# Optimization experiments

Hardware: AMD Instinct MI355X
Metric: run time of the kernel (lower is better)

Reference implementation:

```python
import jax, jax.numpy as jnp
import numpy as np

N = 8192
DIM = 128


def setup_inputs() -> dict:
    key = jax.random.key(0)
    k1, k2 = jax.random.split(key)
    mapping = jax.random.normal(k1, (N, DIM), dtype=jnp.float32)
    # Cost matrix of the finite metric: symmetric, strictly positive off-diagonal,
    # zero diagonal (the module adds eye to the denominator to handle the diagonal).
    Draw = jax.random.uniform(k2, (N, N), dtype=jnp.float32) * 2.0 + 0.1
    D = 0.5 * (Draw + Draw.T)
    D = D * (1.0 - jnp.eye(N, dtype=jnp.float32))
    return {"mapping": mapping, "D": D}


def reference(mapping, D):
    # Pairwise Euclidean distances via GEMM formulation (||a||^2 - 2ab + ||b||^2)
    # instead of materializing the O(N^2 * dim) broadcast difference.
    n = D.shape[0]
    sq = jnp.sum(mapping * mapping, axis=-1)               # [N]
    gram = mapping @ mapping.T                             # [N, N]
    d2 = sq[:, None] + sq[None, :] - 2.0 * gram            # [N, N]
    d2 = jnp.maximum(d2, 0.0)
    # safe sqrt (exact 0 on the diagonal, matching torch.norm forward)
    pos = d2 > 0
    d = jnp.sqrt(jnp.where(pos, d2, 1.0)) * pos
    ratio = jnp.abs(d - D) / (D + jnp.eye(n, dtype=D.dtype))
    return jnp.sum(ratio) / (n * n - n)
```

## Files before the change

### kernel.cpp

```cpp
#include <hip/hip_runtime.h>
#include <math.h>

#define NN 8192
#define DIM 128
#define TS 32
#define NSTRIP (NN / TS)
#define TOTTILES (NSTRIP * (NSTRIP + 1) / 2)
#define TPW 4
#define NWAVE (TOTTILES / TPW)
#define NBLOCKS (NWAVE / 4)

typedef short bf16x8 __attribute__((ext_vector_type(8)));
typedef float f32x4 __attribute__((ext_vector_type(4)));

__device__ inline unsigned short f2bf(float x) {
    unsigned u = __float_as_uint(x);
    unsigned r = u + 0x7FFFu + ((u >> 16) & 1u);
    return (unsigned short)(r >> 16);
}

__global__ void pack_kernel(const float* __restrict__ m, unsigned short* __restrict__ buf2) {
    const int t = threadIdx.x, l = t & 63;
    const int W = blockIdx.x * 4 + (t >> 6);
    const int g = W >> 2, kq = W & 3;
    const int row = g * 16 + (l & 15);
    const int k0 = kq * 32 + (l >> 4) * 8;
    const float* src = m + (size_t)row * DIM + k0;
    float4 v0 = *reinterpret_cast<const float4*>(src);
    float4 v1 = *reinterpret_cast<const float4*>(src + 4);
    float f[8] = {v0.x, v0.y, v0.z, v0.w, v1.x, v1.y, v1.z, v1.w};
    union { ushort4 u4[2]; unsigned short us[8]; } o;
#pragma unroll
    for (int q = 0; q < 8; ++q) o.us[q] = f2bf(f[q]);
    unsigned short* dst = buf2 + (size_t)W * 512 + l * 8;
    *reinterpret_cast<ushort4*>(dst) = o.u4[0];
    *reinterpret_cast<ushort4*>(dst + 4) = o.u4[1];
}

__global__ void sq_kernel(const float* __restrict__ mapping, float* __restrict__ sq) {
    int i = blockIdx.x * blockDim.x + threadIdx.x;
    if (i < NN) {
        const float4* row = reinterpret_cast<const float4*>(mapping + (size_t)i * DIM);
        float s = 0.f;
#pragma unroll
        for (int q = 0; q < DIM / 4; ++q) {
            float4 v = row[q];
            s += v.x * v.x + v.y * v.y + v.z * v.z + v.w * v.w;
        }
        sq[i] = s;
    }
}

__global__ __launch_bounds__(256, 3) void dist_kernel(const unsigned short* __restrict__ buf2,
                                                      const float* __restrict__ D,
                                                      const float* __restrict__ sq,
                                                      float* __restrict__ partials) {
    __shared__ float smem[4][1024];
    __shared__ float wred[4];

    const int t = threadIdx.x, l = t & 63, w = t >> 6;
    const int b = blockIdx.x;
    const int nb = (b & 7) * (NBLOCKS / 8) + (b >> 3);
    const int W = nb * 4 + w;

    int idx0 = __builtin_amdgcn_readfirstlane(W * TPW);
    int si = 0, base = 0;
    while (idx0 >= base + (NSTRIP - si)) { base += NSTRIP - si; ++si; }
    int cj = si + (idx0 - base);

    const int l15 = l & 15, l4 = l >> 4, l7 = l & 7, l3 = l >> 3;
    float* sm = smem[w];

    f32x4 dc[4];
#pragma unroll
    for (int k = 0; k < 4; ++k)
        dc[k] = *reinterpret_cast<const f32x4*>(
            D + (size_t)(si * TS + l3 + 8 * k) * NN + cj * TS + l7 * 4);

    bf16x8 af[2][4];
#pragma unroll
    for (int it = 0; it < 2; ++it)
#pragma unroll
        for (int kq = 0; kq < 4; ++kq)
            af[it][kq] = *(const bf16x8*)(buf2 + (size_t)((si * 2 + it) * 4 + kq) * 512 + l * 8);

    float tsum = 0.f;

#pragma unroll
    for (int tt = 0; tt < TPW; ++tt) {
        int nsi = si, ncj = cj + 1;
        if (ncj == NSTRIP) { nsi = si + 1; ncj = nsi; }
        if (tt == TPW - 1) { nsi = si; ncj = cj; }

        bf16x8 bf[2][4];
#pragma unroll
        for (int jt = 0; jt < 2; ++jt)
#pragma unroll
            for (int kq = 0; kq < 4; ++kq)
                bf[jt][kq] = *(const bf16x8*)(buf2 + (size_t)((cj * 2 + jt) * 4 + kq) * 512 + l * 8);
        float sqa[4];
#pragma unroll
        for (int k = 0; k < 4; ++k) sqa[k] = sq[si * TS + l3 + 8 * k];
        f32x4 sqb = *reinterpret_cast<const f32x4*>(sq + cj * TS + l7 * 4);

        f32x4 dn[4];
#pragma unroll
        for (int k = 0; k < 4; ++k)
            dn[k] = *reinterpret_cast<const f32x4*>(
                D + (size_t)(nsi * TS + l3 + 8 * k) * NN + ncj * TS + l7 * 4);
        __builtin_amdgcn_sched_barrier(0);

        f32x4 acc[2][2] = {};
#pragma unroll
        for (int kq = 0; kq < 4; ++kq)
#pragma unroll
            for (int it = 0; it < 2; ++it)
#pragma unroll
                for (int jt = 0; jt < 2; ++jt)
                    acc[it][jt] = __builtin_amdgcn_mfma_f32_16x16x32_bf16(
                        bf[jt][kq], af[it][kq], acc[it][jt], 0, 0, 0);

#pragma unroll
        for (int it = 0; it < 2; ++it)
#pragma unroll
            for (int jt = 0; jt < 2; ++jt) {
                const int R = it * 16 + l15;
                const int cbytes = (jt * 64 + l4 * 16) ^ ((R & 7) << 4);
                *reinterpret_cast<f32x4*>((char*)&sm[R * 32] + cbytes) = acc[it][jt];
            }
        f32x4 gv[4];
#pragma unroll
        for (int k = 0; k < 4; ++k) {
            const int R = l3 + 8 * k;
            const int cbytes = (l7 * 16) ^ ((R & 7) << 4);
            gv[k] = *reinterpret_cast<const f32x4*>((char*)&sm[R * 32] + cbytes);
        }

        float lsum = 0.f;
#pragma unroll
        for (int k = 0; k < 4; ++k) {
            const int a = si * TS + l3 + 8 * k;
#pragma unroll
            for (int c = 0; c < 4; ++c) {
                const int bcol = cj * TS + l7 * 4 + c;
                float d2 = sqa[k] + sqb[c] - 2.f * gv[k][c];
                float d = d2 > 0.f ? sqrtf(d2) : 0.f;
                float Dv = dc[k][c];
                if (a != bcol) lsum += __fdividef(fabsf(d - Dv), Dv);
            }
        }
        tsum += (si == cj) ? lsum : 2.f * lsum;

#pragma unroll
        for (int k = 0; k < 4; ++k) dc[k] = dn[k];
        ++cj;
        if (cj == NSTRIP) {
            ++si; cj = si;
            if (tt != TPW - 1) {
#pragma unroll
                for (int it = 0; it < 2; ++it)
#pragma unroll
                    for (int kq = 0; kq < 4; ++kq)
                        af[it][kq] = *(const bf16x8*)(buf2 + (size_t)((si * 2 + it) * 4 + kq) * 512 + l * 8);
            }
        }
    }

    for (int off = 32; off > 0; off >>= 1) tsum += __shfl_down(tsum, off, 64);
    __syncthreads();
    if (l == 0) wred[w] = tsum;
    __syncthreads();
    if (t == 0) partials[b] = (wred[0] + wred[1]) + (wred[2] + wred[3]);
}

__global__ void reduce_kernel(const float* __restrict__ partials, float* __restrict__ out) {
    __shared__ double sm[256];
    const int t = threadIdx.x;
    double s = 0.0;
    for (int i = t; i < NBLOCKS; i += 256) s += (double)partials[i];
    sm[t] = s;
    __syncthreads();
    for (int off = 128; off > 0; off >>= 1) {
        if (t < off) sm[t] += sm[t + off];
        __syncthreads();
    }
    if (t == 0) out[0] = (float)(sm[0] / ((double)NN * (double)NN - (double)NN));
}

extern "C" void kernel_launch(void* const* d_in, const int* in_sizes, int n_in,
                              void* d_out, int out_size, void* d_ws, size_t ws_size,
                              hipStream_t stream) {
    const float* mapping = (const float*)d_in[0];
    const float* D       = (const float*)d_in[1];
    float* out = (float*)d_out;

    unsigned short* buf2 = (unsigned short*)d_ws;
    float* sq            = (float*)(buf2 + NN * DIM);
    float* partials      = sq + NN;

    pack_kernel<<<512, 256, 0, stream>>>(mapping, buf2);
    sq_kernel<<<NN / 256, 256, 0, stream>>>(mapping, sq);
    dist_kernel<<<NBLOCKS, 256, 0, stream>>>(buf2, D, sq, partials);
    reduce_kernel<<<1, 256, 0, stream>>>(partials, out);
}
```

Before: 74.03 us.

## Prefetch all D tiles upfront and split diagonal/off-diagonal epilogue paths

Precomputes the tile coordinates for all four tiles handled by a wave and issues every D-tile load at kernel start, instead of prefetching one tile ahead. This exposes more memory-level parallelism on the dominant D stream. The A fragments and row norms are now reloaded only when the strip changes. The epilogue is split so off-diagonal tiles skip the per-element index compare, and diagonal tiles sum only the upper triangle with factor 2. The cost is more live registers (64 floats for D), which may reduce occupancy under launch_bounds(256,3).

```diff
diff --git a/kernel.cpp b/kernel.cpp
--- a/kernel.cpp
+++ b/kernel.cpp
@@ -67,48 +67,59 @@
     int si = 0, base = 0;
     while (idx0 >= base + (NSTRIP - si)) { base += NSTRIP - si; ++si; }
     int cj = si + (idx0 - base);
+    int sit[TPW], cjt[TPW];
+#pragma unroll
+    for (int tt = 0; tt < TPW; ++tt) {
+        sit[tt] = si; cjt[tt] = cj;
+        ++cj;
+        if (cj == NSTRIP) { ++si; cj = si; }
+    }
 
     const int l15 = l & 15, l4 = l >> 4, l7 = l & 7, l3 = l >> 3;
     float* sm = smem[w];
 
-    f32x4 dc[4];
+    f32x4 dall[TPW][4];
 #pragma unroll
     for (int k = 0; k < 4; ++k)
-        dc[k] = *reinterpret_cast<const f32x4*>(
-            D + (size_t)(si * TS + l3 + 8 * k) * NN + cj * TS + l7 * 4);
+#pragma unroll
+        for (int tt = 0; tt < TPW; ++tt)
+            dall[tt][k] = *reinterpret_cast<const f32x4*>(
+                D + (size_t)(sit[tt] * TS + l3 + 8 * k) * NN + cjt[tt] * TS + l7 * 4);
+    __builtin_amdgcn_sched_barrier(0);
 
     bf16x8 af[2][4];
+    float sqa[4];
 #pragma unroll
     for (int it = 0; it < 2; ++it)
 #pragma unroll
         for (int kq = 0; kq < 4; ++kq)
-            af[it][kq] = *(const bf16x8*)(buf2 + (size_t)((si * 2 + it) * 4 + kq) * 512 + l * 8);
+            af[it][kq] = *(const bf16x8*)(buf2 + (size_t)((sit[0] * 2 + it) * 4 + kq) * 512 + l * 8);
+#pragma unroll
+    for (int k = 0; k < 4; ++k) sqa[k] = sq[sit[0] * TS + l3 + 8 * k];
 
     float tsum = 0.f;
 
 #pragma unroll
     for (int tt = 0; tt < TPW; ++tt) {
-        int nsi = si, ncj = cj + 1;
-        if (ncj == NSTRIP) { nsi = si + 1; ncj = nsi; }
-        if (tt == TPW - 1) { nsi = si; ncj = cj; }
-
-        bf16x8 bf[2][4];
+        const int csi = sit[tt], ccj = cjt[tt];
+
+        if (tt > 0 && sit[tt] != sit[tt - 1]) {
+#pragma unroll
+            for (int it = 0; it < 2; ++it)
+#pragma unroll
+                for (int kq = 0; kq < 4; ++kq)
+                    af[it][kq] = *(const bf16x8*)(buf2 + (size_t)((csi * 2 + it) * 4 + kq) * 512 + l * 8);
+#pragma unroll
+            for (int k = 0; k < 4; ++k) sqa[k] = sq[csi * TS + l3 + 8 * k];
+        }
+
+        bf16x8 bfr[2][4];
 #pragma unroll
         for (int jt = 0; jt < 2; ++jt)
 #pragma unroll
             for (int kq = 0; kq < 4; ++kq)
-                bf[jt][kq] = *(const bf16x8*)(buf2 + (size_t)((cj * 2 + jt) * 4 + kq) * 512 + l * 8);
-        float sqa[4];
-#pragma unroll
-        for (int k = 0; k < 4; ++k) sqa[k] = sq[si * TS + l3 + 8 * k];
-        f32x4 sqb = *reinterpret_cast<const f32x4*>(sq + cj * TS + l7 * 4);
-
-        f32x4 dn[4];
-#pragma unroll
-        for (int k = 0; k < 4; ++k)
-            dn[k] = *reinterpret_cast<const f32x4*>(
-                D + (size_t)(nsi * TS + l3 + 8 * k) * NN + ncj * TS + l7 * 4);
-        __builtin_amdgcn_sched_barrier(0);
+                bfr[jt][kq] = *(const bf16x8*)(buf2 + (size_t)((ccj * 2 + jt) * 4 + kq) * 512 + l * 8);
+        f32x4 sqb = *reinterpret_cast<const f32x4*>(sq + ccj * TS + l7 * 4);
 
         f32x4 acc[2][2] = {};
 #pragma unroll
@@ -118,7 +129,7 @@
 #pragma unroll
                 for (int jt = 0; jt < 2; ++jt)
                     acc[it][jt] = __builtin_amdgcn_mfma_f32_16x16x32_bf16(
-                        bf[jt][kq], af[it][kq], acc[it][jt], 0, 0, 0);
+                        bfr[jt][kq], af[it][kq], acc[it][jt], 0, 0, 0);
 
 #pragma unroll
         for (int it = 0; it < 2; ++it)
@@ -136,33 +147,36 @@
             gv[k] = *reinterpret_cast<const f32x4*>((char*)&sm[R * 32] + cbytes);
         }
 
-        float lsum = 0.f;
-#pragma unroll
-        for (int k = 0; k < 4; ++k) {
-            const int a = si * TS + l3 + 8 * k;
-#pragma unroll
-            for (int c = 0; c < 4; ++c) {
-                const int bcol = cj * TS + l7 * 4 + c;
-                float d2 = sqa[k] + sqb[c] - 2.f * gv[k][c];
-                float d = d2 > 0.f ? sqrtf(d2) : 0.f;
-                float Dv = dc[k][c];
-                if (a != bcol) lsum += __fdividef(fabsf(d - Dv), Dv);
+        if (csi != ccj) {
+            float lsum = 0.f;
+#pragma unroll
+            for (int k = 0; k < 4; ++k) {
+                const float sa = sqa[k];
+#pragma unroll
+                for (int c = 0; c < 4; ++c) {
+                    float d2 = fmaf(-2.f, gv[k][c], sa + sqb[c]);
+                    float d = sqrtf(fmaxf(d2, 0.f));
+                    float Dv = dall[tt][k][c];
+                    lsum += __fdividef(fabsf(d - Dv), Dv);
+                }
             }
-        }
-        tsum += (si == cj) ? lsum : 2.f * lsum;
-
-#pragma unroll
-        for (int k = 0; k < 4; ++k) dc[k] = dn[k];
-        ++cj;
-        if (cj == NSTRIP) {
-            ++si; cj = si;
-            if (tt != TPW - 1) {
-#pragma unroll
-                for (int it = 0; it < 2; ++it)
-#pragma unroll
-                    for (int kq = 0; kq < 4; ++kq)
-                        af[it][kq] = *(const bf16x8*)(buf2 + (size_t)((si * 2 + it) * 4 + kq) * 512 + l * 8);
+            tsum += 2.f * lsum;
+        } else {
+            float lsum = 0.f;
+#pragma unroll
+            for (int k = 0; k < 4; ++k) {
+                const int a = csi * TS + l3 + 8 * k;
+                const float sa = sqa[k];
+#pragma unroll
+                for (int c = 0; c < 4; ++c) {
+                    const int bcol = ccj * TS + l7 * 4 + c;
+                    float d2 = fmaf(-2.f, gv[k][c], sa + sqb[c]);
+                    float d = sqrtf(fmaxf(d2, 0.f));
+                    float Dv = dall[tt][k][c];
+                    if (a < bcol) lsum += __fdividef(fabsf(d - Dv), Dv);
+                }
             }
+            tsum += 2.f * lsum;
         }
     }
 
```

Result: no change. 73.34 us (-0.9%).

## Restructure distance kernel into row-strip work items without LDS transpose

Applied to the files above, without the earlier changes.

The kernel now assigns each wave a 16-row strip and a strided set of 64-column tiles across the upper triangle, with work items pulled by a persistent grid-stride loop. Each lane consumes MFMA accumulator values directly in their native layout, loading D and sq values to match, which removes the shared-memory transpose and its barriers. A-fragments are loaded once per item and reused across many column tiles, and D is prefetched one tile ahead. Diagonal tiles mask elementwise with j>i and every contribution is doubled. The trade-off is more items (8192 partials to reduce) and possibly uneven load per item.

```diff
diff --git a/kernel.cpp b/kernel.cpp
--- a/kernel.cpp
+++ b/kernel.cpp
@@ -3,12 +3,11 @@
 
 #define NN 8192
 #define DIM 128
-#define TS 32
-#define NSTRIP (NN / TS)
-#define TOTTILES (NSTRIP * (NSTRIP + 1) / 2)
-#define TPW 4
-#define NWAVE (TOTTILES / TPW)
-#define NBLOCKS (NWAVE / 4)
+#define NG 512
+#define NCT 128
+#define NITEMS (NG * 16)
+#define NBLOCKS 768
+#define NWT (NBLOCKS * 4)
 
 typedef short bf16x8 __attribute__((ext_vector_type(8)));
 typedef float f32x4 __attribute__((ext_vector_type(4)));
@@ -55,129 +54,104 @@
                                                       const float* __restrict__ D,
                                                       const float* __restrict__ sq,
                                                       float* __restrict__ partials) {
-    __shared__ float smem[4][1024];
-    __shared__ float wred[4];
+    const int t = threadIdx.x, l = t & 63;
+    const int W = blockIdx.x * 4 + (t >> 6);
 
-    const int t = threadIdx.x, l = t & 63, w = t >> 6;
-    const int b = blockIdx.x;
-    const int nb = (b & 7) * (NBLOCKS / 8) + (b >> 3);
-    const int W = nb * 4 + w;
+    const int l15 = l & 15;
+    const int colq = (l >> 4) * 4;
 
-    int idx0 = __builtin_amdgcn_readfirstlane(W * TPW);
-    int si = 0, base = 0;
-    while (idx0 >= base + (NSTRIP - si)) { base += NSTRIP - si; ++si; }
-    int cj = si + (idx0 - base);
+    int item = W;
+    while (item < NITEMS) {
+        const int g = item >> 4, p = item & 15;
+        int cj = (g >> 2) + p;
+        if (cj >= NCT) {
+            if (l == 0) partials[item] = 0.f;
+            item += NWT;
+            continue;
+        }
 
-    const int l15 = l & 15, l4 = l >> 4, l7 = l & 7, l3 = l >> 3;
-    float* sm = smem[w];
+        const int i_row = g * 16 + l15;
+        const int cdiag = g >> 2;
 
-    f32x4 dc[4];
-#pragma unroll
-    for (int k = 0; k < 4; ++k)
-        dc[k] = *reinterpret_cast<const f32x4*>(
-            D + (size_t)(si * TS + l3 + 8 * k) * NN + cj * TS + l7 * 4);
-
-    bf16x8 af[2][4];
-#pragma unroll
-    for (int it = 0; it < 2; ++it)
+        bf16x8 af[4];
 #pragma unroll
         for (int kq = 0; kq < 4; ++kq)
-            af[it][kq] = *(const bf16x8*)(buf2 + (size_t)((si * 2 + it) * 4 + kq) * 512 + l * 8);
+            af[kq] = *(const bf16x8*)(buf2 + (size_t)(g * 4 + kq) * 512 + l * 8);
+        const float sa = sq[i_row];
 
-    float tsum = 0.f;
+        f32x4 dc[4], sbc[4];
+#pragma unroll
+        for (int s = 0; s < 4; ++s) {
+            dc[s] = *reinterpret_cast<const f32x4*>(D + (size_t)i_row * NN + cj * 64 + s * 16 + colq);
+            sbc[s] = *reinterpret_cast<const f32x4*>(sq + cj * 64 + s * 16 + colq);
+        }
+
+        float psum = 0.f;
+        for (; cj < NCT; cj += 16) {
+            const int ncj = cj + 16;
+
+            bf16x8 bfr[4][4];
+#pragma unroll
+            for (int s = 0; s < 4; ++s)
+#pragma unroll
+                for (int kq = 0; kq < 4; ++kq)
+                    bfr[s][kq] = *(const bf16x8*)(buf2 + (size_t)((cj * 4 + s) * 4 + kq) * 512 + l * 8);
+
+            f32x4 dn[4], sbn[4];
+            if (ncj < NCT) {
+#pragma unroll
+                for (int s = 0; s < 4; ++s) {
+                    dn[s] = *reinterpret_cast<const f32x4*>(D + (size_t)i_row * NN + ncj * 64 + s * 16 + colq);
+                    sbn[s] = *reinterpret_cast<const f32x4*>(sq + ncj * 64 + s * 16 + colq);
+                }
+            }
 
 #pragma unroll
-    for (int tt = 0; tt < TPW; ++tt) {
-        int nsi = si, ncj = cj + 1;
-        if (ncj == NSTRIP) { nsi = si + 1; ncj = nsi; }
-        if (tt == TPW - 1) { nsi = si; ncj = cj; }
+            for (int s = 0; s < 4; ++s) {
+                f32x4 acc = {};
+#pragma unroll
+                for (int kq = 0; kq < 4; ++kq)
+                    acc = __builtin_amdgcn_mfma_f32_16x16x32_bf16(bfr[s][kq], af[kq], acc, 0, 0, 0);
+                if (cj != cdiag) {
+#pragma unroll
+                    for (int r = 0; r < 4; ++r) {
+                        float d2 = fmaf(-2.f, acc[r], sa + sbc[s][r]);
+                        float d = sqrtf(fmaxf(d2, 0.f));
+                        float Dv = dc[s][r];
+                        psum += __fdividef(fabsf(d - Dv), Dv);
+                    }
+                } else {
+#pragma unroll
+                    for (int r = 0; r < 4; ++r) {
+                        const int j = cj * 64 + s * 16 + colq + r;
+                        if (j > i_row) {
+                            float d2 = fmaf(-2.f, acc[r], sa + sbc[s][r]);
+                            float d = sqrtf(fmaxf(d2, 0.f));
+                            float Dv = dc[s][r];
+                            psum += __fdividef(fabsf(d - Dv), Dv);
+                        }
+                    }
+                }
+            }
 
-        bf16x8 bf[2][4];
+            if (ncj < NCT) {
 #pragma unroll
-        for (int jt = 0; jt < 2; ++jt)
-#pragma unroll
-            for (int kq = 0; kq < 4; ++kq)
-                bf[jt][kq] = *(const bf16x8*)(buf2 + (size_t)((cj * 2 + jt) * 4 + kq) * 512 + l * 8);
-        float sqa[4];
-#pragma unroll
-        for (int k = 0; k < 4; ++k) sqa[k] = sq[si * TS + l3 + 8 * k];
-        f32x4 sqb = *reinterpret_cast<const f32x4*>(sq + cj * TS + l7 * 4);
-
-        f32x4 dn[4];
-#pragma unroll
-        for (int k = 0; k < 4; ++k)
-            dn[k] = *reinterpret_cast<const f32x4*>(
-                D + (size_t)(nsi * TS + l3 + 8 * k) * NN + ncj * TS + l7 * 4);
-        __builtin_amdgcn_sched_barrier(0);
-
-        f32x4 acc[2][2] = {};
-#pragma unroll
-        for (int kq = 0; kq < 4; ++kq)
-#pragma unroll
-            for (int it = 0; it < 2; ++it)
-#pragma unroll
-                for (int jt = 0; jt < 2; ++jt)
-                    acc[it][jt] = __builtin_amdgcn_mfma_f32_16x16x32_bf16(
-                        bf[jt][kq], af[it][kq], acc[it][jt], 0, 0, 0);
-
-#pragma unroll
-        for (int it = 0; it < 2; ++it)
-#pragma unroll
-            for (int jt = 0; jt < 2; ++jt) {
-                const int R = it * 16 + l15;
-                const int cbytes = (jt * 64 + l4 * 16) ^ ((R & 7) << 4);
-                *reinterpret_cast<f32x4*>((char*)&sm[R * 32] + cbytes) = acc[it][jt];
+                for (int s = 0; s < 4; ++s) { dc[s] = dn[s]; sbc[s] = sbn[s]; }
             }
-        f32x4 gv[4];
-#pragma unroll
-        for (int k = 0; k < 4; ++k) {
-            const int R = l3 + 8 * k;
-            const int cbytes = (l7 * 16) ^ ((R & 7) << 4);
-            gv[k] = *reinterpret_cast<const f32x4*>((char*)&sm[R * 32] + cbytes);
         }
 
-        float lsum = 0.f;
-#pragma unroll
-        for (int k = 0; k < 4; ++k) {
-            const int a = si * TS + l3 + 8 * k;
-#pragma unroll
-            for (int c = 0; c < 4; ++c) {
-                const int bcol = cj * TS + l7 * 4 + c;
-                float d2 = sqa[k] + sqb[c] - 2.f * gv[k][c];
-                float d = d2 > 0.f ? sqrtf(d2) : 0.f;
-                float Dv = dc[k][c];
-                if (a != bcol) lsum += __fdividef(fabsf(d - Dv), Dv);
-            }
-        }
-        tsum += (si == cj) ? lsum : 2.f * lsum;
+        for (int off = 32; off > 0; off >>= 1) psum += __shfl_down(psum, off, 64);
+        if (l == 0) partials[item] = 2.f * psum;
 
-#pragma unroll
-        for (int k = 0; k < 4; ++k) dc[k] = dn[k];
-        ++cj;
-        if (cj == NSTRIP) {
-            ++si; cj = si;
-            if (tt != TPW - 1) {
-#pragma unroll
-                for (int it = 0; it < 2; ++it)
-#pragma unroll
-                    for (int kq = 0; kq < 4; ++kq)
-                        af[it][kq] = *(const bf16x8*)(buf2 + (size_t)((si * 2 + it) * 4 + kq) * 512 + l * 8);
-            }
-        }
+        item += NWT;
     }
-
-    for (int off = 32; off > 0; off >>= 1) tsum += __shfl_down(tsum, off, 64);
-    __syncthreads();
-    if (l == 0) wred[w] = tsum;
-    __syncthreads();
-    if (t == 0) partials[b] = (wred[0] + wred[1]) + (wred[2] + wred[3]);
 }
 
 __global__ void reduce_kernel(const float* __restrict__ partials, float* __restrict__ out) {
     __shared__ double sm[256];
     const int t = threadIdx.x;
     double s = 0.0;
-    for (int i = t; i < NBLOCKS; i += 256) s += (double)partials[i];
+    for (int i = t; i < NITEMS; i += 256) s += (double)partials[i];
     sm[t] = s;
     __syncthreads();
     for (int off = 128; off > 0; off >>= 1) {
```

Result: no change. 75.41 us (+1.9%).
